# Optimization experiments

Hardware: AMD Instinct MI355X
Metric: run time of the kernel (lower is better)

Reference implementation:

```python
import jax, jax.numpy as jnp
import numpy as np

N_QUBITS = 8
N_CYCLES = 4
N_LAYERS = 2  # log2(8) - 1
B = 65536

CNOT = jnp.array([[1, 0, 0, 0],
                  [0, 1, 0, 0],
                  [0, 0, 0, 1],
                  [0, 0, 1, 0]], dtype=jnp.complex64)


def apply_gate(state, U, wires):
    """Apply a (2^k x 2^k) gate U on the given wires of state (B, 2,2,...,2).
    Wire 0 is the leftmost (most significant) qubit axis."""
    k = len(wires)
    src = [w + 1 for w in wires]
    dst = list(range(1, 1 + k))
    st = jnp.moveaxis(state, src, dst)
    shp = st.shape
    st = st.reshape(shp[0], 2 ** k, -1)
    st = jnp.einsum('ij,bjr->bir', U, st)
    return jnp.moveaxis(st.reshape(shp), dst, src)


def apply_ry(state, q, angles):
    """Batched RY(angle) on qubit q; angles has shape (B,)."""
    st = jnp.moveaxis(state, q + 1, 1)  # (B, 2, rest...)
    c = jnp.cos(0.5 * angles).reshape((-1,) + (1,) * (st.ndim - 2))
    s = jnp.sin(0.5 * angles).reshape((-1,) + (1,) * (st.ndim - 2))
    s0, s1 = st[:, 0], st[:, 1]
    new = jnp.stack([c * s0 - s * s1, s * s0 + c * s1], axis=1)
    return jnp.moveaxis(new, 1, q + 1)


def crx_mat(theta):
    c = (jnp.cos(0.5 * theta) + 0j).astype(jnp.complex64)
    s = (-1j * jnp.sin(0.5 * theta)).astype(jnp.complex64)
    one = jnp.ones((), jnp.complex64)
    zero = jnp.zeros((), jnp.complex64)
    return jnp.stack([
        jnp.stack([one, zero, zero, zero]),
        jnp.stack([zero, one, zero, zero]),
        jnp.stack([zero, zero, c, s]),
        jnp.stack([zero, zero, s, c]),
    ])


def u3_mat(p):
    th, ph, lm = p[0], p[1], p[2]
    ct = (jnp.cos(0.5 * th) + 0j).astype(jnp.complex64)
    st = (jnp.sin(0.5 * th) + 0j).astype(jnp.complex64)
    el = jnp.exp(1j * lm).astype(jnp.complex64)
    ep = jnp.exp(1j * ph).astype(jnp.complex64)
    return jnp.stack([
        jnp.stack([ct, -el * st]),
        jnp.stack([ep * st, ep * el * ct]),
    ])


def expval_z(state, q):
    st = jnp.moveaxis(state, q + 1, 1)
    p = (st.real ** 2 + st.imag ** 2).reshape(st.shape[0], 2, -1).sum(-1)
    return p[:, 0] - p[:, 1]


def _forward(x, crx_theta, u3_params, w1, b1, w2, b2):
    b = x.shape[0]
    # |0...0> initial state, shape (B, 2,2,...,2)
    state = jnp.zeros((b, 2 ** N_QUBITS), jnp.complex64).at[:, 0].set(1.0)
    state = state.reshape((b,) + (2,) * N_QUBITS)
    # encoder: data re-uploading RY angle encoding + CNOT ring, n_cycles times
    for _ in range(N_CYCLES):
        for q in range(N_QUBITS):
            state = apply_ry(state, q, x[:, q])
        for q in range(N_QUBITS):
            state = apply_gate(state, CNOT, [q, (q + 1) % N_QUBITS])
    # QCNN conv/pool layers with shared weights per layer
    active = list(range(N_QUBITS))
    for layer in range(N_LAYERS):
        U = crx_mat(crx_theta[layer])
        for i in range(0, len(active) - 1, 2):
            state = apply_gate(state, U, [active[i], active[i + 1]])
        for i in range(1, len(active) - 1, 2):
            state = apply_gate(state, U, [active[i], active[i + 1]])
        remain = active[1::2]
        # mid-circuit expval in the original is discarded and does not alter state
        V = u3_mat(u3_params[layer])
        for q in remain:
            state = apply_gate(state, V, [q])
        active = remain
    feats = jnp.stack([expval_z(state, q) for q in active], axis=1)  # (B, 2)
    h = jnp.tanh(feats @ w1 + b1)
    return jax.nn.sigmoid(h @ w2 + b2)  # (B, 1)


def setup_inputs() -> dict:
    key = jax.random.key(0)
    ks = jax.random.split(key, 6)
    return {
        'x': jax.random.normal(ks[0], (B, N_QUBITS), jnp.float32),
        'crx_theta': jax.random.normal(ks[1], (N_LAYERS,), jnp.float32),
        'u3_params': jax.random.normal(ks[2], (N_LAYERS, 3), jnp.float32),
        'w1': jax.random.normal(ks[3], (2, 10), jnp.float32) * 0.5,
        'b1': jnp.zeros((10,), jnp.float32),
        'w2': jax.random.normal(ks[4], (10, 1), jnp.float32) * 0.5,
        'b2': jnp.zeros((1,), jnp.float32),
    }


def reference(x, crx_theta, u3_params, w1, b1, w2, b2):
    return _forward(x, crx_theta, u3_params, w1, b1, w2, b2)
```

## Files before the change

kernel.cpp:

```cpp
#include <hip/hip_runtime.h>


#define NQ 8
#define NE 2
#define FRAG_OFF 0
#define UR_OFF   65536
#define UI_OFF   98304
#define ANG_OFF  131072

typedef _Float16 h2 __attribute__((ext_vector_type(2)));
typedef _Float16 h8 __attribute__((ext_vector_type(8)));
typedef float    f4 __attribute__((ext_vector_type(4)));

__device__ __forceinline__ float h2f(h2 v){ return __builtin_bit_cast(float, v); }
__device__ __forceinline__ h2 f2h(float v){ return __builtin_bit_cast(h2, v); }
__device__ __forceinline__ h2 u2h(unsigned u){ return __builtin_bit_cast(h2, u); }
__device__ __forceinline__ unsigned h2u(h2 v){ return __builtin_bit_cast(unsigned, v); }
__device__ __forceinline__ h2 negh(h2 v){ return u2h(h2u(v) ^ 0x80008000u); }
__device__ __forceinline__ h2 mk(float x){ return __builtin_bit_cast(h2, __builtin_amdgcn_cvt_pkrtz(x,x)); }
__device__ __forceinline__ h2 mk2(float a, float b){ return __builtin_bit_cast(h2, __builtin_amdgcn_cvt_pkrtz(a,b)); }
__device__ __forceinline__ h2 fma2h(h2 a, h2 b, h2 c){ return __builtin_elementwise_fma(a,b,c); }
__device__ __forceinline__ h2 swp(h2 v){ return __builtin_shufflevector(v,v,1,0); }

template<int CTRL>
__device__ __forceinline__ float dppf(float v){
    return __int_as_float(__builtin_amdgcn_mov_dpp(__float_as_int(v), CTRL, 0xF, 0xF, true));
}
template<int M>
__device__ __forceinline__ float sx(float v){
    if constexpr (M==1)       return dppf<0xB1>(v);
    else if constexpr (M==2)  return dppf<0x4E>(v);
    else if constexpr (M==32) return __shfl_xor(v, 32, 64);
    else return __int_as_float(__builtin_amdgcn_ds_swizzle(__float_as_int(v), (M<<10)|0x1F));
}
__device__ __forceinline__ void cmulh(h2&R, h2&I, h2 C, h2 S, h2 nS){
    h2 nR = fma2h(C, R, nS*I);
    I = fma2h(C, I, S*R);
    R = nR;
}

#define FOR_E _Pragma("unroll") for (int e = 0; e < NE; ++e)

#define RINGF() do { FOR_E { \
    h2 TA = pb ? B[e] : A[e]; \
    h2 TS = pb ? A[e] : B[e]; \
    int V0 = (int)__builtin_amdgcn_perm(h2u(TS), h2u(TA), 0x07060100u); \
    int V1 = (int)__builtin_amdgcn_perm(h2u(TA), h2u(TS), 0x07060100u); \
    unsigned r0 = (unsigned)__builtin_amdgcn_ds_bpermute(ba0, V0); \
    unsigned r1 = (unsigned)__builtin_amdgcn_ds_bpermute(ba1, V1); \
    A[e] = u2h(__builtin_amdgcn_perm(r1, r0, 0x07060100u)); \
    B[e] = u2h(__builtin_amdgcn_perm(r1, r0, 0x05040302u)); } \
} while(0)

struct P2C {
    h2 cc0,sn0,nsn0, cc1,sn1,nsn1;
    h2 uct0,ust0,nust0,usv0;
    h2 uct1,ust1,nust1;
    h2 cl1,sl1,nsl1, cp1,sp1,nsp1;
    h2 E0,E1,E2,E3,G2,G3;
    h2 Clm,Slm,nSlm,Cph,Sph,nSph;
    h2 tu1,tu3,tu5;
};

__device__ __forceinline__ P2C load_consts(const unsigned* wsu, int l){
    P2C K;
    const bool L4=(l>>4)&1, L2=(l>>2)&1, L0=l&1;
    K.cc0=u2h(wsu[0]); K.sn0=u2h(wsu[1]); K.cc1=u2h(wsu[2]); K.sn1=u2h(wsu[3]);
    K.nsn0=negh(K.sn0); K.nsn1=negh(K.sn1);
    K.uct0=u2h(wsu[4]); K.ust0=u2h(wsu[5]); K.nust0=u2h(wsu[6]); K.usv0=u2h(wsu[7]);
    K.uct1=u2h(wsu[8]); K.ust1=u2h(wsu[9]); K.nust1=u2h(wsu[10]);
    K.cl1=u2h(wsu[11]); K.sl1=u2h(wsu[12]); K.nsl1=negh(K.sl1);
    K.cp1=u2h(wsu[13]); K.sp1=u2h(wsu[14]); K.nsp1=negh(K.sp1);
    K.E0=u2h(wsu[15]); K.E1=u2h(wsu[16]); K.E2=u2h(wsu[17]);
    K.E3=u2h(wsu[18]); K.G2=u2h(wsu[19]); K.G3=u2h(wsu[20]);
    const int ki = (int)L4 + (int)L2 + (int)L0;
    K.Clm=u2h(wsu[24+ki*4+0]); K.Slm=u2h(wsu[24+ki*4+1]);
    K.Cph=u2h(wsu[24+ki*4+2]); K.Sph=u2h(wsu[24+ki*4+3]);
    K.nSlm=negh(K.Slm); K.nSph=negh(K.Sph);
    K.tu1 = L4 ? K.ust0 : K.nust0;
    K.tu3 = L2 ? K.ust0 : K.nust0;
    K.tu5 = L0 ? K.ust0 : K.nust0;
    return K;
}

#define SHF4(M) h2 oRA[NE], oIA[NE], oRB[NE], oIB[NE]; \
    FOR_E { oRA[e]=f2h(sx<M>(h2f(RA[e]))); oIA[e]=f2h(sx<M>(h2f(IA[e]))); \
            oRB[e]=f2h(sx<M>(h2f(RB[e]))); oIB[e]=f2h(sx<M>(h2f(IB[e]))); }
#define CRX_LL(CSH, M, cc, sn, nsn) do { \
    const bool ct = (l >> (CSH)) & 1; \
    SHF4(M) \
    if (ct) { FOR_E { \
        RA[e] = fma2h(cc, RA[e], (sn)*oIA[e]); IA[e] = fma2h(cc, IA[e], (nsn)*oRA[e]); \
        RB[e] = fma2h(cc, RB[e], (sn)*oIB[e]); IB[e] = fma2h(cc, IB[e], (nsn)*oRB[e]); } } \
} while(0)
#define RYC0(M, T) do { \
    SHF4(M) \
    FOR_E { \
    RA[e] = fma2h(K.uct0, RA[e], (T)*oRA[e]); IA[e] = fma2h(K.uct0, IA[e], (T)*oIA[e]); \
    RB[e] = fma2h(K.uct0, RB[e], (T)*oRB[e]); IB[e] = fma2h(K.uct0, IB[e], (T)*oIB[e]); } \
} while(0)

__device__ __forceinline__ void phase2run(const int l, const P2C& K,
    const h2* A, const h2* B, h2* RA, h2* RB, h2* IA, h2* IB)
{
    const bool L5=(l>>5)&1, L2=(l>>2)&1, L0=l&1;
    FOR_E { RA[e]=A[e]; RB[e]=B[e]; IA[e]=(h2){0,0}; IB[e]=(h2){0,0}; }

    {   h2 oA[NE], oB[NE];
        FOR_E { oA[e]=f2h(sx<16>(h2f(RA[e]))); oB[e]=f2h(sx<16>(h2f(RB[e]))); }
        if (L5){ FOR_E {
            IA[e] = K.nsn0*oA[e]; RA[e] = K.cc0*RA[e];
            IB[e] = K.nsn0*oB[e]; RB[e] = K.cc0*RB[e]; } }
    }
    CRX_LL(3, 4, K.cc0, K.sn0, K.nsn0);
    CRX_LL(1, 1, K.cc0, K.sn0, K.nsn0);
    FOR_E {
        h2 oI = swp(IB[e]), oR = swp(RB[e]);
        RB[e] = fma2h(K.cc0, RB[e], K.sn0*oI);
        IB[e] = fma2h(K.cc0, IB[e], K.nsn0*oR);
    }
    CRX_LL(4, 8, K.cc0, K.sn0, K.nsn0);
    CRX_LL(2, 2, K.cc0, K.sn0, K.nsn0);
    if (L0) { FOR_E {
        h2 nRA = fma2h(K.cc0, RA[e], K.sn0*IB[e]);
        h2 nRB = fma2h(K.cc0, RB[e], K.sn0*IA[e]);
        h2 nIA = fma2h(K.cc0, IA[e], K.nsn0*RB[e]);
        h2 nIB = fma2h(K.cc0, IB[e], K.nsn0*RA[e]);
        RA[e]=nRA; RB[e]=nRB; IA[e]=nIA; IB[e]=nIB; } }
    FOR_E { cmulh(RA[e],IA[e],K.Clm,K.Slm,K.nSlm); cmulh(RB[e],IB[e],K.Clm,K.Slm,K.nSlm); }
    RYC0(16, K.tu1);
    RYC0(4,  K.tu3);
    RYC0(1,  K.tu5);
    FOR_E {
        h2 sA=swp(RA[e]), sB=swp(RB[e]), tA=swp(IA[e]), tB=swp(IB[e]);
        RA[e] = fma2h(K.uct0, RA[e], K.usv0*sA); RB[e] = fma2h(K.uct0, RB[e], K.usv0*sB);
        IA[e] = fma2h(K.uct0, IA[e], K.usv0*tA); IB[e] = fma2h(K.uct0, IB[e], K.usv0*tB);
    }
    FOR_E { cmulh(RA[e],IA[e],K.Cph,K.Sph,K.nSph); cmulh(RB[e],IB[e],K.Cph,K.Sph,K.nSph); }

    CRX_LL(4, 4, K.cc1, K.sn1, K.nsn1);
    if (L0) { FOR_E {
        h2 sIA=swp(IA[e]), sRA=swp(RA[e]), sIB=swp(IB[e]), sRB=swp(RB[e]);
        RA[e] = fma2h(K.cc1, RA[e], K.sn1*sIA); IA[e] = fma2h(K.cc1, IA[e], K.nsn1*sRA);
        RB[e] = fma2h(K.cc1, RB[e], K.sn1*sIB); IB[e] = fma2h(K.cc1, IB[e], K.nsn1*sRB); } }
    CRX_LL(2, 1, K.cc1, K.sn1, K.nsn1);
    {
        if (L2){ FOR_E { cmulh(RA[e],IA[e],K.cl1,K.sl1,K.nsl1); cmulh(RB[e],IB[e],K.cl1,K.sl1,K.nsl1); } }
        h2 T = L2 ? K.ust1 : K.nust1;
        SHF4(4)
        FOR_E {
            RA[e] = fma2h(K.uct1, RA[e], T*oRA[e]); IA[e] = fma2h(K.uct1, IA[e], T*oIA[e]);
            RB[e] = fma2h(K.uct1, RB[e], T*oRB[e]); IB[e] = fma2h(K.uct1, IB[e], T*oIB[e]);
        }
        if (L2){ FOR_E { cmulh(RA[e],IA[e],K.cp1,K.sp1,K.nsp1); cmulh(RB[e],IB[e],K.cp1,K.sp1,K.nsp1); } }
    }
    FOR_E {
        h2 sR=swp(RA[e]), sI=swp(IA[e]);
        h2 nR = fma2h(K.E3,sI, fma2h(K.E2,IA[e], fma2h(K.E1,sR, K.E0*RA[e])));
        h2 nI = fma2h(K.G3,sR, fma2h(K.G2,RA[e], fma2h(K.E1,sI, K.E0*IA[e])));
        RA[e]=nR; IA[e]=nI;
        h2 sR2=swp(RB[e]), sI2=swp(IB[e]);
        h2 nR2 = fma2h(K.E3,sI2, fma2h(K.E2,IB[e], fma2h(K.E1,sR2, K.E0*RB[e])));
        h2 nI2 = fma2h(K.G3,sR2, fma2h(K.G2,RB[e], fma2h(K.E1,sI2, K.E0*IB[e])));
        RB[e]=nR2; IB[e]=nI2;
    }
}

__global__ __launch_bounds__(256) void qcnn_angles(
    const float* __restrict__ x, float* __restrict__ ang, int Btot)
{
    const int e = blockIdx.x*256 + threadIdx.x;
    if (e >= Btot) return;
    const float4* xv = (const float4*)(x + e*NQ);
    float4 xa=xv[0], xb=xv[1];
    float a[8]={xa.x,xa.y,xa.z,xa.w,xb.x,xb.y,xb.z,xb.w};
    float c[8], s[8];
#pragma unroll
    for(int q=0;q<8;++q) __sincosf(0.5f*a[q], &s[q], &c[q]);
    float4* ov = (float4*)(ang + e*16);
    ov[0] = make_float4(c[0],c[1],c[2],c[3]);
    ov[1] = make_float4(c[4],c[5],c[6],c[7]);
    ov[2] = make_float4(s[0],s[1],s[2],s[3]);
    ov[3] = make_float4(s[4],s[5],s[6],s[7]);
}

__global__ __launch_bounds__(1024) void qcnn_prep_u(
    const float* __restrict__ crx, const float* __restrict__ u3p,
    unsigned* __restrict__ ws)
{
    __shared__ unsigned cws[48];
    if (threadIdx.x == 0){
        auto PK=[](float lo, float hi)->unsigned{
            unsigned a=__builtin_bit_cast(unsigned short,(_Float16)lo);
            unsigned b=__builtin_bit_cast(unsigned short,(_Float16)hi);
            return a | (b<<16);
        };
        float sc0,cc0,sc1,cc1;
        __sincosf(0.5f*crx[0],&sc0,&cc0);
        __sincosf(0.5f*crx[1],&sc1,&cc1);
        cws[0]=PK(cc0,cc0); cws[1]=PK(sc0,sc0); cws[2]=PK(cc1,cc1); cws[3]=PK(sc1,sc1);
        float th0=u3p[0], ph0=u3p[1], lm0=u3p[2];
        float ust0,uct0; __sincosf(0.5f*th0,&ust0,&uct0);
        cws[4]=PK(uct0,uct0); cws[5]=PK(ust0,ust0); cws[6]=PK(-ust0,-ust0); cws[7]=PK(-ust0,ust0);
        float th1=u3p[3], ph1=u3p[4], lm1=u3p[5];
        float ust1,uct1; __sincosf(0.5f*th1,&ust1,&uct1);
        float sl1,cl1;   __sincosf(lm1,&sl1,&cl1);
        float sp1,cp1;   __sincosf(ph1,&sp1,&cp1);
        cws[8]=PK(uct1,uct1); cws[9]=PK(ust1,ust1); cws[10]=PK(-ust1,-ust1);
        cws[11]=PK(cl1,cl1); cws[12]=PK(sl1,sl1); cws[13]=PK(cp1,cp1); cws[14]=PK(sp1,sp1);
        float cpl1=cp1*cl1-sp1*sl1, spl1=sp1*cl1+cp1*sl1;
        float u01r=-ust1*cl1, u01i=-ust1*sl1;
        float u10r= ust1*cp1, u10i= ust1*sp1;
        float u11r= uct1*cpl1, u11i= uct1*spl1;
        cws[15]=PK(uct1,u11r); cws[16]=PK(u01r,u10r); cws[17]=PK(0.f,-u11i);
        cws[18]=PK(-u01i,-u10i); cws[19]=PK(0.f,u11i); cws[20]=PK(u01i,u10i);
        for(int k=0;k<4;++k){
            float kf=(float)k, sA,cA,sB,cB,sA2,cA2,sB2,cB2;
            __sincosf(lm0*kf,      &sA,&cA);
            __sincosf(lm0*(kf+1.f),&sB,&cB);
            __sincosf(ph0*kf,      &sA2,&cA2);
            __sincosf(ph0*(kf+1.f),&sB2,&cB2);
            unsigned* q = cws + 24 + k*4;
            q[0]=PK(cA,cB); q[1]=PK(sA,sB); q[2]=PK(cA2,cB2); q[3]=PK(sA2,sB2);
        }
    }
    __syncthreads();

    const int l = threadIdx.x & 63;
    const int w = threadIdx.x >> 6;
    const P2C K = load_consts(cws, l);
    const bool pb = __builtin_popcount(l) & 1;
    const int ba0 = (((l&32)|((l^(l>>1))&31)) << 2);
    const int ba1 = ba0 ^ (48<<2);

    const int j0 = blockIdx.x*32 + w*2;
    h2 A[NE], B[NE];
    FOR_E {
        A[e]=(h2){0,0}; B[e]=(h2){0,0};
        const int j = j0 + e;
        if (l == (j >> 2)){
            const int slot = j & 3;
            const _Float16 one = (_Float16)1.f;
            if      (slot==0) A[e].x = one;
            else if (slot==1) A[e].y = one;
            else if (slot==2) B[e].x = one;
            else              B[e].y = one;
        }
    }
    RINGF();
    h2 RA[NE], RB[NE], IA[NE], IB[NE];
    phase2run(l, K, A, B, RA, RB, IA, IB);
    FOR_E {
        const int j = j0 + e;
        *(uint2*)(ws + UR_OFF + j*128 + l*2) = make_uint2(h2u(RA[e]), h2u(RB[e]));
        *(uint2*)(ws + UI_OFF + j*128 + l*2) = make_uint2(h2u(IA[e]), h2u(IB[e]));
    }
}

__global__ void qcnn_prep_frag(unsigned* __restrict__ ws){
    const int T = blockIdx.x*256 + threadIdx.x;
    const int chunk = T >> 6, l = T & 63;
    const int ct = chunk >> 4, ri = (chunk >> 3) & 1, ks = chunk & 7;
    const unsigned short* U = (const unsigned short*)(ws + (ri ? UI_OFF : UR_OFF));
    const int n = ct*16 + (l & 15);
    const int g = l >> 4;
    unsigned d[4];
#pragma unroll
    for (int p = 0; p < 4; ++p){
        const int k0 = ks*32 + g*8 + 2*p;
        unsigned lo = U[k0*256 + n];
        unsigned hi = U[(k0+1)*256 + n];
        d[p] = lo | (hi << 16);
    }
    uint4 v; v.x=d[0]; v.y=d[1]; v.z=d[2]; v.w=d[3];
    *(uint4*)(ws + FRAG_OFF + chunk*256 + l*4) = v;
}

__global__ __launch_bounds__(1024) void qcnn_kernel(
    const unsigned* __restrict__ wsu,
    const float* __restrict__ w1,
    const float* __restrict__ b1,
    const float* __restrict__ w2,
    const float* __restrict__ b2,
    float* __restrict__ out,
    int Btot)
{
    __shared__ __align__(16) unsigned char Sl[16*1024];
    __shared__ __align__(16) float parts[2][32][16];
    const int tid = threadIdx.x;
    const int l = tid & 63;
    const int w = tid >> 6;
    const int eblk = blockIdx.x * 32;
    const int e0 = eblk + w*NE;
    const bool L5=(l>>5)&1, L4=(l>>4)&1, L3=(l>>3)&1, L2=(l>>2)&1, L1=(l>>1)&1, L0=l&1;

    const bool pb = __builtin_popcount(l) & 1;
    const int ba0 = (((l&32)|((l^(l>>1))&31)) << 2);
    const int ba1 = ba0 ^ (48<<2);

    const bool bits[6]={L5,L4,L3,L2,L1,L0};
    unsigned sm[6];
#pragma unroll
    for(int q=0;q<6;++q) sm[q] = bits[q] ? 0u : 0x80008000u;

    h2 cH[NE][6], tsH[NE][6];
    h2 c6h[NE], s6h[NE], ns6h[NE], c7h[NE], sv7h[NE];
    h2 A[NE], B[NE];
    const float* angv = (const float*)(wsu + ANG_OFF);
    FOR_E {
        const int ee = (e0 + e < Btot) ? (e0 + e) : (Btot - 1);
        const float4* av = (const float4*)(angv + ee*16);
        float4 ca=av[0], cb=av[1], sa=av[2], sb=av[3];
        float cq[8]={ca.x,ca.y,ca.z,ca.w,cb.x,cb.y,cb.z,cb.w};
        float sq[8]={sa.x,sa.y,sa.z,sa.w,sb.x,sb.y,sb.z,sb.w};
#pragma unroll
        for(int q=0;q<6;++q){
            cH[e][q]=mk(cq[q]);
            tsH[e][q]=u2h(h2u(mk(sq[q])) ^ sm[q]);
        }
        c6h[e]=mk(cq[6]); s6h[e]=mk(sq[6]); ns6h[e]=negh(s6h[e]);
        c7h[e]=mk(cq[7]); sv7h[e]=mk2(-sq[7], sq[7]);
        float pl = (L5?sq[0]:cq[0])*(L4?sq[1]:cq[1])*(L3?sq[2]:cq[2])
                 * (L2?sq[3]:cq[3])*(L1?sq[4]:cq[4])*(L0?sq[5]:cq[5]);
        float pc6=pl*cq[6], ps6=pl*sq[6];
        A[e] = mk2(pc6*cq[7], pc6*sq[7]);
        B[e] = mk2(ps6*cq[7], ps6*sq[7]);
    }

#define RY_L(q, M) do { FOR_E { \
    h2 oA = f2h(sx<M>(h2f(A[e]))), oB = f2h(sx<M>(h2f(B[e]))); \
    A[e] = fma2h(cH[e][q], A[e], tsH[e][q]*oA); \
    B[e] = fma2h(cH[e][q], B[e], tsH[e][q]*oB); } \
} while(0)

    RINGF();
#pragma unroll
    for(int cyc=0;cyc<3;++cyc){
        RY_L(0,32); RY_L(1,16); RY_L(2,8); RY_L(3,4); RY_L(4,2); RY_L(5,1);
        FOR_E { h2 nA = fma2h(c6h[e], A[e], ns6h[e]*B[e]);
                h2 nB = fma2h(s6h[e], A[e], c6h[e]*B[e]);
                A[e]=nA; B[e]=nB; }
        FOR_E { A[e] = fma2h(c7h[e], A[e], sv7h[e]*swp(A[e]));
                B[e] = fma2h(c7h[e], B[e], sv7h[e]*swp(B[e])); }
        if (cyc < 2) RINGF();
    }

    FOR_E {
        const int r = w*NE + e;
        const int mblk = r >> 4, rr = r & 15;
        const int ks = l >> 3, g = (l >> 1) & 3, p = l & 1;
        const unsigned off = (unsigned)(((mblk*8 + ks) << 10)
                             + (((rr + 16*g) ^ ks) << 4) + (p << 3));
        *(uint2*)(Sl + off) = make_uint2(h2u(A[e]), h2u(B[e]));
    }
    __syncthreads();

    f4 aR0={0,0,0,0}, aI0={0,0,0,0}, aR1={0,0,0,0}, aI1={0,0,0,0};
    const unsigned* frag = wsu + FRAG_OFF;
#pragma unroll
    for (int ks = 0; ks < 8; ++ks){
        h8 a0 = *(const h8*)(Sl + ((     ks) << 10) + ((l ^ ks) << 4));
        h8 a1 = *(const h8*)(Sl + ((8 +  ks) << 10) + ((l ^ ks) << 4));
        h8 br = *(const h8*)(frag + (w*16 +     ks)*256 + l*4);
        h8 bi = *(const h8*)(frag + (w*16 + 8 + ks)*256 + l*4);
        aR0 = __builtin_amdgcn_mfma_f32_16x16x32_f16(a0, br, aR0, 0, 0, 0);
        aR1 = __builtin_amdgcn_mfma_f32_16x16x32_f16(a1, br, aR1, 0, 0, 0);
        aI0 = __builtin_amdgcn_mfma_f32_16x16x32_f16(a0, bi, aI0, 0, 0, 0);
        aI1 = __builtin_amdgcn_mfma_f32_16x16x32_f16(a1, bi, aI1, 0, 0, 0);
    }

    const float s3 = (w & 1) ? -1.f : 1.f;
    const float s7 = (l & 1) ? -1.f : 1.f;
    const int g = l >> 4;
    float f0a[4], f1a[4], f0b[4], f1b[4];
#pragma unroll
    for (int r = 0; r < 4; ++r){
        float nv0 = fmaf(aR0[r], aR0[r], aI0[r]*aI0[r]);
        float nv1 = fmaf(aR1[r], aR1[r], aI1[r]*aI1[r]);
        f0a[r] = s3*nv0; f1a[r] = s7*nv0;
        f0b[r] = s3*nv1; f1b[r] = s7*nv1;
    }
#pragma unroll
    for (int r = 0; r < 4; ++r){
        f0a[r] += sx<1>(f0a[r]); f0a[r] += sx<2>(f0a[r]); f0a[r] += sx<4>(f0a[r]); f0a[r] += sx<8>(f0a[r]);
        f1a[r] += sx<1>(f1a[r]); f1a[r] += sx<2>(f1a[r]); f1a[r] += sx<4>(f1a[r]); f1a[r] += sx<8>(f1a[r]);
        f0b[r] += sx<1>(f0b[r]); f0b[r] += sx<2>(f0b[r]); f0b[r] += sx<4>(f0b[r]); f0b[r] += sx<8>(f0b[r]);
        f1b[r] += sx<1>(f1b[r]); f1b[r] += sx<2>(f1b[r]); f1b[r] += sx<4>(f1b[r]); f1b[r] += sx<8>(f1b[r]);
    }
    if ((l & 15) == 0){
        const int rb = g*4;
#pragma unroll
        for (int r = 0; r < 4; ++r){
            parts[0][rb+r]   [w] = f0a[r];
            parts[1][rb+r]   [w] = f1a[r];
            parts[0][16+rb+r][w] = f0b[r];
            parts[1][16+rb+r][w] = f1b[r];
        }
    }
    __syncthreads();

    if (tid < 512){
        const int elem = tid >> 4, k = tid & 15;
        const float4* p0 = (const float4*)&parts[0][elem][0];
        const float4* p1 = (const float4*)&parts[1][elem][0];
        float4 u0=p0[0], u1=p0[1], u2=p0[2], u3=p0[3];
        float4 v0=p1[0], v1=p1[1], v2=p1[2], v3=p1[3];
        float F0 = ((u0.x+u0.y)+(u0.z+u0.w)) + ((u1.x+u1.y)+(u1.z+u1.w))
                 + ((u2.x+u2.y)+(u2.z+u2.w)) + ((u3.x+u3.y)+(u3.z+u3.w));
        float F1 = ((v0.x+v0.y)+(v0.z+v0.w)) + ((v1.x+v1.y)+(v1.z+v1.w))
                 + ((v2.x+v2.y)+(v2.z+v2.w)) + ((v3.x+v3.y)+(v3.z+v3.w));
        float contrib = 0.0f;
        if (k < 10){
            float z = fmaf(F0, w1[k], fmaf(F1, w1[10+k], b1[k]));
            float ex = __expf(2.0f*z);
            contrib = ((ex-1.0f)/(ex+1.0f)) * w2[k];
        }
        contrib += sx<1>(contrib);
        contrib += sx<2>(contrib);
        contrib += sx<4>(contrib);
        contrib += sx<8>(contrib);
        if (k == 0 && eblk + elem < Btot){
            out[eblk + elem] = 1.0f/(1.0f + __expf(-(contrib + b2[0])));
        }
    }
}

extern "C" void kernel_launch(void* const* d_in, const int* in_sizes, int n_in,
                              void* d_out, int out_size, void* d_ws, size_t ws_size,
                              hipStream_t stream) {
    const float* x   = (const float*)d_in[0];
    const float* crx = (const float*)d_in[1];
    const float* u3p = (const float*)d_in[2];
    const float* w1  = (const float*)d_in[3];
    const float* b1  = (const float*)d_in[4];
    const float* w2  = (const float*)d_in[5];
    const float* b2  = (const float*)d_in[6];
    float* out = (float*)d_out;
    unsigned* ws = (unsigned*)d_ws;

    const int B = in_sizes[0] / NQ;
    hipLaunchKernelGGL(qcnn_angles, dim3((B+255)/256), dim3(256), 0, stream,
                       x, (float*)(ws + ANG_OFF), B);
    hipLaunchKernelGGL(qcnn_prep_u,    dim3(8),  dim3(1024), 0, stream, crx, u3p, ws);
    hipLaunchKernelGGL(qcnn_prep_frag, dim3(64), dim3(256),  0, stream, ws);
    const int grid = (B + 31) / 32;
    hipLaunchKernelGGL(qcnn_kernel, dim3(grid), dim3(1024), 0, stream,
                       ws, w1, b1, w2, b2, out, B);
}
```

Baseline: 121.9 us.

## Process 64 batch elements per block, reusing each unitary fragment across four MFMA tiles

```diff
diff --git a/kernel.cpp b/kernel.cpp
--- a/kernel.cpp
+++ b/kernel.cpp
@@ -285,13 +285,12 @@
     float* __restrict__ out,
     int Btot)
 {
-    __shared__ __align__(16) unsigned char Sl[16*1024];
-    __shared__ __align__(16) float parts[2][32][16];
+    __shared__ __align__(16) unsigned char Sl[32*1024];
+    __shared__ float parts[2][64][17];
     const int tid = threadIdx.x;
     const int l = tid & 63;
     const int w = tid >> 6;
-    const int eblk = blockIdx.x * 32;
-    const int e0 = eblk + w*NE;
+    const int eblk = blockIdx.x * 64;
     const bool L5=(l>>5)&1, L4=(l>>4)&1, L3=(l>>3)&1, L2=(l>>2)&1, L1=(l>>1)&1, L0=l&1;
 
     const bool pb = __builtin_popcount(l) & 1;
@@ -303,29 +302,29 @@
 #pragma unroll
     for(int q=0;q<6;++q) sm[q] = bits[q] ? 0u : 0x80008000u;
 
-    h2 cH[NE][6], tsH[NE][6];
-    h2 c6h[NE], s6h[NE], ns6h[NE], c7h[NE], sv7h[NE];
-    h2 A[NE], B[NE];
     const float* angv = (const float*)(wsu + ANG_OFF);
-    FOR_E {
-        const int ee = (e0 + e < Btot) ? (e0 + e) : (Btot - 1);
-        const float4* av = (const float4*)(angv + ee*16);
-        float4 ca=av[0], cb=av[1], sa=av[2], sb=av[3];
-        float cq[8]={ca.x,ca.y,ca.z,ca.w,cb.x,cb.y,cb.z,cb.w};
-        float sq[8]={sa.x,sa.y,sa.z,sa.w,sb.x,sb.y,sb.z,sb.w};
-#pragma unroll
-        for(int q=0;q<6;++q){
-            cH[e][q]=mk(cq[q]);
-            tsH[e][q]=u2h(h2u(mk(sq[q])) ^ sm[q]);
-        }
-        c6h[e]=mk(cq[6]); s6h[e]=mk(sq[6]); ns6h[e]=negh(s6h[e]);
-        c7h[e]=mk(cq[7]); sv7h[e]=mk2(-sq[7], sq[7]);
-        float pl = (L5?sq[0]:cq[0])*(L4?sq[1]:cq[1])*(L3?sq[2]:cq[2])
-                 * (L2?sq[3]:cq[3])*(L1?sq[4]:cq[4])*(L0?sq[5]:cq[5]);
-        float pc6=pl*cq[6], ps6=pl*sq[6];
-        A[e] = mk2(pc6*cq[7], pc6*sq[7]);
-        B[e] = mk2(ps6*cq[7], ps6*sq[7]);
-    }
+
+#define LOAD_ANG(dst, rbase) do { FOR_E { \
+    int ee = eblk + (rbase) + e; if (ee >= Btot) ee = Btot - 1; \
+    const float4* av = (const float4*)(angv + ee*16); \
+    dst[e][0]=av[0]; dst[e][1]=av[1]; dst[e][2]=av[2]; dst[e][3]=av[3]; } \
+} while(0)
+
+#define BUILD_COEF(av) FOR_E { \
+    float4 ca=av[e][0], cb=av[e][1], sa=av[e][2], sb=av[e][3]; \
+    float cq[8]={ca.x,ca.y,ca.z,ca.w,cb.x,cb.y,cb.z,cb.w}; \
+    float sq[8]={sa.x,sa.y,sa.z,sa.w,sb.x,sb.y,sb.z,sb.w}; \
+    _Pragma("unroll") for(int q=0;q<6;++q){ \
+        cH[e][q]=mk(cq[q]); \
+        tsH[e][q]=u2h(h2u(mk(sq[q])) ^ sm[q]); } \
+    c6h[e]=mk(cq[6]); s6h[e]=mk(sq[6]); ns6h[e]=negh(s6h[e]); \
+    c7h[e]=mk(cq[7]); sv7h[e]=mk2(-sq[7], sq[7]); \
+    float pl = (L5?sq[0]:cq[0])*(L4?sq[1]:cq[1])*(L3?sq[2]:cq[2]) \
+             * (L2?sq[3]:cq[3])*(L1?sq[4]:cq[4])*(L0?sq[5]:cq[5]); \
+    float pc6=pl*cq[6], ps6=pl*sq[6]; \
+    A[e] = mk2(pc6*cq[7], pc6*sq[7]); \
+    B[e] = mk2(ps6*cq[7], ps6*sq[7]); \
+}
 
 #define RY_L(q, M) do { FOR_E { \
     h2 oA = f2h(sx<M>(h2f(A[e]))), oB = f2h(sx<M>(h2f(B[e]))); \
@@ -333,82 +332,95 @@
     B[e] = fma2h(cH[e][q], B[e], tsH[e][q]*oB); } \
 } while(0)
 
-    RINGF();
-#pragma unroll
-    for(int cyc=0;cyc<3;++cyc){
-        RY_L(0,32); RY_L(1,16); RY_L(2,8); RY_L(3,4); RY_L(4,2); RY_L(5,1);
-        FOR_E { h2 nA = fma2h(c6h[e], A[e], ns6h[e]*B[e]);
-                h2 nB = fma2h(s6h[e], A[e], c6h[e]*B[e]);
-                A[e]=nA; B[e]=nB; }
-        FOR_E { A[e] = fma2h(c7h[e], A[e], sv7h[e]*swp(A[e]));
-                B[e] = fma2h(c7h[e], B[e], sv7h[e]*swp(B[e])); }
-        if (cyc < 2) RINGF();
-    }
-
-    FOR_E {
-        const int r = w*NE + e;
-        const int mblk = r >> 4, rr = r & 15;
-        const int ks = l >> 3, g = (l >> 1) & 3, p = l & 1;
-        const unsigned off = (unsigned)(((mblk*8 + ks) << 10)
-                             + (((rr + 16*g) ^ ks) << 4) + (p << 3));
-        *(uint2*)(Sl + off) = make_uint2(h2u(A[e]), h2u(B[e]));
+#define LADDER() do { \
+    RINGF(); \
+    _Pragma("unroll") for(int cyc=0;cyc<3;++cyc){ \
+        RY_L(0,32); RY_L(1,16); RY_L(2,8); RY_L(3,4); RY_L(4,2); RY_L(5,1); \
+        FOR_E { h2 nA = fma2h(c6h[e], A[e], ns6h[e]*B[e]); \
+                h2 nB = fma2h(s6h[e], A[e], c6h[e]*B[e]); \
+                A[e]=nA; B[e]=nB; } \
+        FOR_E { A[e] = fma2h(c7h[e], A[e], sv7h[e]*swp(A[e])); \
+                B[e] = fma2h(c7h[e], B[e], sv7h[e]*swp(B[e])); } \
+        if (cyc < 2) RINGF(); \
+    } \
+} while(0)
+
+#define STAGE(rbase) do { FOR_E { \
+    const int r = (rbase) + e; \
+    const int mblk = r >> 4, rr = r & 15; \
+    const int ks = l >> 3, g2 = (l >> 1) & 3, pp = l & 1; \
+    const unsigned gran = (unsigned)((rr | (g2<<4)) ^ ks ^ (g2<<1)); \
+    const unsigned off = (unsigned)(((mblk*8 + ks) << 10) | (gran << 4) | (pp << 3)); \
+    *(uint2*)(Sl + off) = make_uint2(h2u(A[e]), h2u(B[e])); } \
+} while(0)
+
+    float4 av0[NE][4], av1[NE][4];
+    LOAD_ANG(av0, w*4);
+    {
+        h2 cH[NE][6], tsH[NE][6];
+        h2 c6h[NE], s6h[NE], ns6h[NE], c7h[NE], sv7h[NE];
+        h2 A[NE], B[NE];
+        BUILD_COEF(av0);
+        LOAD_ANG(av1, w*4 + 2);
+        LADDER();
+        STAGE(w*4);
+    }
+    {
+        h2 cH[NE][6], tsH[NE][6];
+        h2 c6h[NE], s6h[NE], ns6h[NE], c7h[NE], sv7h[NE];
+        h2 A[NE], B[NE];
+        BUILD_COEF(av1);
+        LADDER();
+        STAGE(w*4 + 2);
     }
     __syncthreads();
 
-    f4 aR0={0,0,0,0}, aI0={0,0,0,0}, aR1={0,0,0,0}, aI1={0,0,0,0};
+    f4 aR0={0,0,0,0}, aR1={0,0,0,0}, aR2={0,0,0,0}, aR3={0,0,0,0};
+    f4 aI0={0,0,0,0}, aI1={0,0,0,0}, aI2={0,0,0,0}, aI3={0,0,0,0};
     const unsigned* frag = wsu + FRAG_OFF;
 #pragma unroll
     for (int ks = 0; ks < 8; ++ks){
-        h8 a0 = *(const h8*)(Sl + ((     ks) << 10) + ((l ^ ks) << 4));
-        h8 a1 = *(const h8*)(Sl + ((8 +  ks) << 10) + ((l ^ ks) << 4));
         h8 br = *(const h8*)(frag + (w*16 +     ks)*256 + l*4);
         h8 bi = *(const h8*)(frag + (w*16 + 8 + ks)*256 + l*4);
+        const unsigned ga = (unsigned)((l ^ ks ^ ((l>>4)<<1)) << 4);
+        h8 a0 = *(const h8*)(Sl + ((0*8 + ks) << 10) + ga);
+        h8 a1 = *(const h8*)(Sl + ((1*8 + ks) << 10) + ga);
+        h8 a2 = *(const h8*)(Sl + ((2*8 + ks) << 10) + ga);
+        h8 a3 = *(const h8*)(Sl + ((3*8 + ks) << 10) + ga);
         aR0 = __builtin_amdgcn_mfma_f32_16x16x32_f16(a0, br, aR0, 0, 0, 0);
+        aI0 = __builtin_amdgcn_mfma_f32_16x16x32_f16(a0, bi, aI0, 0, 0, 0);
         aR1 = __builtin_amdgcn_mfma_f32_16x16x32_f16(a1, br, aR1, 0, 0, 0);
-        aI0 = __builtin_amdgcn_mfma_f32_16x16x32_f16(a0, bi, aI0, 0, 0, 0);
         aI1 = __builtin_amdgcn_mfma_f32_16x16x32_f16(a1, bi, aI1, 0, 0, 0);
-    }
-
-    const float s3 = (w & 1) ? -1.f : 1.f;
-    const float s7 = (l & 1) ? -1.f : 1.f;
+        aR2 = __builtin_amdgcn_mfma_f32_16x16x32_f16(a2, br, aR2, 0, 0, 0);
+        aI2 = __builtin_amdgcn_mfma_f32_16x16x32_f16(a2, bi, aI2, 0, 0, 0);
+        aR3 = __builtin_amdgcn_mfma_f32_16x16x32_f16(a3, br, aR3, 0, 0, 0);
+        aI3 = __builtin_amdgcn_mfma_f32_16x16x32_f16(a3, bi, aI3, 0, 0, 0);
+    }
+
     const int g = l >> 4;
-    float f0a[4], f1a[4], f0b[4], f1b[4];
-#pragma unroll
-    for (int r = 0; r < 4; ++r){
-        float nv0 = fmaf(aR0[r], aR0[r], aI0[r]*aI0[r]);
-        float nv1 = fmaf(aR1[r], aR1[r], aI1[r]*aI1[r]);
-        f0a[r] = s3*nv0; f1a[r] = s7*nv0;
-        f0b[r] = s3*nv1; f1b[r] = s7*nv1;
-    }
-#pragma unroll
-    for (int r = 0; r < 4; ++r){
-        f0a[r] += sx<1>(f0a[r]); f0a[r] += sx<2>(f0a[r]); f0a[r] += sx<4>(f0a[r]); f0a[r] += sx<8>(f0a[r]);
-        f1a[r] += sx<1>(f1a[r]); f1a[r] += sx<2>(f1a[r]); f1a[r] += sx<4>(f1a[r]); f1a[r] += sx<8>(f1a[r]);
-        f0b[r] += sx<1>(f0b[r]); f0b[r] += sx<2>(f0b[r]); f0b[r] += sx<4>(f0b[r]); f0b[r] += sx<8>(f0b[r]);
-        f1b[r] += sx<1>(f1b[r]); f1b[r] += sx<2>(f1b[r]); f1b[r] += sx<4>(f1b[r]); f1b[r] += sx<8>(f1b[r]);
-    }
-    if ((l & 15) == 0){
-        const int rb = g*4;
-#pragma unroll
-        for (int r = 0; r < 4; ++r){
-            parts[0][rb+r]   [w] = f0a[r];
-            parts[1][rb+r]   [w] = f1a[r];
-            parts[0][16+rb+r][w] = f0b[r];
-            parts[1][16+rb+r][w] = f1b[r];
-        }
-    }
+#define REDU(aR, aI, mb) do { \
+    _Pragma("unroll") for (int r = 0; r < 4; ++r){ \
+        float nv = fmaf(aR[r], aR[r], aI[r]*aI[r]); \
+        float o  = sx<1>(nv); \
+        float v0 = nv + o, v1 = nv - o; \
+        v0 += sx<2>(v0); v1 += sx<2>(v1); \
+        v0 += sx<4>(v0); v1 += sx<4>(v1); \
+        v0 += sx<8>(v0); v1 += sx<8>(v1); \
+        if ((l & 15) == 0){ \
+            parts[0][(mb)*16 + g*4 + r][w] = v0; \
+            parts[1][(mb)*16 + g*4 + r][w] = v1; } \
+    } \
+} while(0)
+    REDU(aR0, aI0, 0); REDU(aR1, aI1, 1); REDU(aR2, aI2, 2); REDU(aR3, aI3, 3);
     __syncthreads();
 
-    if (tid < 512){
+    {
         const int elem = tid >> 4, k = tid & 15;
-        const float4* p0 = (const float4*)&parts[0][elem][0];
-        const float4* p1 = (const float4*)&parts[1][elem][0];
-        float4 u0=p0[0], u1=p0[1], u2=p0[2], u3=p0[3];
-        float4 v0=p1[0], v1=p1[1], v2=p1[2], v3=p1[3];
-        float F0 = ((u0.x+u0.y)+(u0.z+u0.w)) + ((u1.x+u1.y)+(u1.z+u1.w))
-                 + ((u2.x+u2.y)+(u2.z+u2.w)) + ((u3.x+u3.y)+(u3.z+u3.w));
-        float F1 = ((v0.x+v0.y)+(v0.z+v0.w)) + ((v1.x+v1.y)+(v1.z+v1.w))
-                 + ((v2.x+v2.y)+(v2.z+v2.w)) + ((v3.x+v3.y)+(v3.z+v3.w));
+        float F0 = parts[0][elem][k];
+        float F1 = parts[1][elem][k];
+        F0 = __int_as_float(__float_as_int(F0) ^ ((k & 1) << 31));
+        F0 += sx<1>(F0); F0 += sx<2>(F0); F0 += sx<4>(F0); F0 += sx<8>(F0);
+        F1 += sx<1>(F1); F1 += sx<2>(F1); F1 += sx<4>(F1); F1 += sx<8>(F1);
         float contrib = 0.0f;
         if (k < 10){
             float z = fmaf(F0, w1[k], fmaf(F1, w1[10+k], b1[k]));
@@ -443,7 +455,7 @@
                        x, (float*)(ws + ANG_OFF), B);
     hipLaunchKernelGGL(qcnn_prep_u,    dim3(8),  dim3(1024), 0, stream, crx, u3p, ws);
     hipLaunchKernelGGL(qcnn_prep_frag, dim3(64), dim3(256),  0, stream, ws);
-    const int grid = (B + 31) / 32;
+    const int grid = (B + 63) / 64;
     hipLaunchKernelGGL(qcnn_kernel, dim3(grid), dim3(1024), 0, stream,
                        ws, w1, b1, w2, b2, out, B);
 }
```

Measured after the change: 166.6 us. +36.7%, slower.
